# Performance work log

Measured on AMD Instinct MI355X. Metric: run time of the kernel, lower is better.

Reference implementation:

```python
import jax, jax.numpy as jnp
import numpy as np

N_NODES = 50000
N_EDGES = 1_600_000
N_HEADS = 8
IN_DIM = 512
OUT_DIM = 64
LRELU_ALPHA = 0.2


def setup_inputs() -> dict:
    key = jax.random.key(0)
    k1, k2, k3, k4, k5 = jax.random.split(key, 5)
    x = jax.random.normal(k1, (N_NODES, IN_DIM), dtype=jnp.float32)
    # glorot-ish scale for weights
    W = jax.random.normal(k2, (N_HEADS, IN_DIM, OUT_DIM), dtype=jnp.float32) * (1.0 / np.sqrt(IN_DIM))
    att_w = jax.random.normal(k3, (N_HEADS, 2 * OUT_DIM), dtype=jnp.float32) * (1.0 / np.sqrt(2 * OUT_DIM))
    src = jax.random.randint(k4, (N_EDGES,), 0, N_NODES, dtype=jnp.int64 if jax.config.read('jax_enable_x64') else jnp.int32).astype(jnp.int32)
    dst = jax.random.randint(k5, (N_EDGES,), 0, N_NODES, dtype=jnp.int32)
    return {"x": x, "W": W, "att_w": att_w, "src": src, "dst": dst}


def reference(x, W, att_w, src, dst):
    # GAT forward (eval mode: dropout=0, bias off, heads concatenated).
    # attention score: leaky_relu([f_src || f_dst] @ a) == leaky_relu(a1.f_src + a2.f_dst)
    outs = []
    for h in range(N_HEADS):
        feat = x @ W[h]                               # [N, F]
        a1 = att_w[h, :OUT_DIM]                       # [F]
        a2 = att_w[h, OUT_DIM:]                       # [F]
        alpha_s = feat @ a1                           # [N]
        alpha_d = feat @ a2                           # [N]
        logit = jax.nn.leaky_relu(alpha_s[src] + alpha_d[dst], LRELU_ALPHA)  # [E]
        # sparse row-wise softmax over segments keyed by src (row index)
        m = jax.ops.segment_max(logit, src, num_segments=N_NODES)
        e = jnp.exp(logit - m[src])
        denom = jax.ops.segment_sum(e, src, num_segments=N_NODES)
        att = e / denom[src]                          # [E]
        # sparse-dense aggregation: out[row] = sum_edges att * feat[col]
        agg = jax.ops.segment_sum(att[:, None] * feat[dst], src, num_segments=N_NODES)  # [N, F]
        outs.append(jax.nn.relu(agg))                 # act per head (average_heads=False)
    return jnp.concatenate(outs, axis=1)              # [N, H*F]
```

## Files before the change

### kernel.cpp

```cpp
#include <hip/hip_runtime.h>
#include <math.h>

#define N_NODES   50000
#define N_EDGES   1600000
#define N_HEADS   8
#define IN_DIM    512
#define OUT_DIM   64
#define FEAT_DIM  512
#define LRELU_A   0.2f
#define M_TILES   391
#define M_PAD     (M_TILES*128)

#define DBLK_SHIFT 11
#define NBLK       25
#define NKEYS      (N_NODES * NBLK)
#define KSCAN_BLK  ((NKEYS + 1023) / 1024)

typedef __attribute__((ext_vector_type(8))) short bf16x8;
typedef __attribute__((ext_vector_type(4))) short bf16x4;
typedef __attribute__((ext_vector_type(4))) float f32x4;

__device__ inline unsigned short f2bf(float f) {
    unsigned int u = __float_as_uint(f);
    u = (u + 0x7FFFu + ((u >> 16) & 1u)) >> 16;
    return (unsigned short)u;
}
__device__ inline float bf2f(short s) {
    return __uint_as_float(((unsigned int)(unsigned short)s) << 16);
}

__global__ __launch_bounds__(256) void convert_x(const float* __restrict__ x,
                                                 unsigned short* __restrict__ xh) {
    int i = blockIdx.x * blockDim.x + threadIdx.x;
    if (i >= N_NODES * IN_DIM / 4) return;
    float4 v = ((const float4*)x)[i];
    ushort4 o;
    o.x = f2bf(v.x); o.y = f2bf(v.y); o.z = f2bf(v.z); o.w = f2bf(v.w);
    ((ushort4*)xh)[i] = o;
}

__global__ __launch_bounds__(256) void prep_b(const float* __restrict__ W,
                                              unsigned short* __restrict__ Bt) {
    int t = blockIdx.x * blockDim.x + threadIdx.x;
    if (t >= FEAT_DIM * IN_DIM) return;
    int n = t >> 9, k = t & 511;
    int h = n >> 6, o = n & 63;
    Bt[t] = f2bf(W[(size_t)h * IN_DIM * OUT_DIM + (size_t)k * OUT_DIM + o]);
}

__global__ __launch_bounds__(256) void gemm_mfma(const unsigned short* __restrict__ xh,
                                                 const unsigned short* __restrict__ Bt,
                                                 unsigned short* __restrict__ feat_h) {
    __shared__ __align__(16) unsigned short As[128 * 32];
    __shared__ __align__(16) unsigned short Bs[128 * 32];
    const int t    = threadIdx.x;
    const int wid  = t >> 6;
    const int lane = t & 63;
    const int m0   = blockIdx.x * 128;
    const int n0   = blockIdx.y * 128;
    const int wm   = (wid >> 1) * 64;
    const int wn   = (wid & 1) * 64;
    const int mr   = lane & 15;
    const int q    = lane >> 4;

    f32x4 acc[4][4];
    #pragma unroll
    for (int i = 0; i < 4; ++i)
        #pragma unroll
        for (int j = 0; j < 4; ++j) acc[i][j] = 0.0f;

    const char* xb = (const char*)xh;
    const char* bb = (const char*)Bt;
    const int o1 = t * 16;         const int row1 = o1 >> 6, kb1 = o1 & 63;
    const int o2 = t * 16 + 4096;  const int row2 = o2 >> 6, kb2 = o2 & 63;
    char* lA1 = ((char*)As) + wid * 1024;
    char* lA2 = ((char*)As) + 4096 + wid * 1024;
    char* lB1 = ((char*)Bs) + wid * 1024;
    char* lB2 = ((char*)Bs) + 4096 + wid * 1024;

    for (int k0 = 0; k0 < IN_DIM; k0 += 32) {
        const int kbyte = k0 * 2;
        __builtin_amdgcn_global_load_lds(
            (const __attribute__((address_space(1))) unsigned int*)(xb + (size_t)(m0 + row1) * (IN_DIM * 2) + kbyte + kb1),
            (__attribute__((address_space(3))) unsigned int*)lA1, 16, 0, 0);
        __builtin_amdgcn_global_load_lds(
            (const __attribute__((address_space(1))) unsigned int*)(xb + (size_t)(m0 + row2) * (IN_DIM * 2) + kbyte + kb2),
            (__attribute__((address_space(3))) unsigned int*)lA2, 16, 0, 0);
        __builtin_amdgcn_global_load_lds(
            (const __attribute__((address_space(1))) unsigned int*)(bb + (size_t)(n0 + row1) * (IN_DIM * 2) + kbyte + kb1),
            (__attribute__((address_space(3))) unsigned int*)lB1, 16, 0, 0);
        __builtin_amdgcn_global_load_lds(
            (const __attribute__((address_space(1))) unsigned int*)(bb + (size_t)(n0 + row2) * (IN_DIM * 2) + kbyte + kb2),
            (__attribute__((address_space(3))) unsigned int*)lB2, 16, 0, 0);
        __syncthreads();

        bf16x8 a[4], b[4];
        #pragma unroll
        for (int i = 0; i < 4; ++i)
            a[i] = *(const bf16x8*)&As[(wm + i * 16 + mr) * 32 + q * 8];
        #pragma unroll
        for (int j = 0; j < 4; ++j)
            b[j] = *(const bf16x8*)&Bs[(wn + j * 16 + mr) * 32 + q * 8];
        #pragma unroll
        for (int i = 0; i < 4; ++i)
            #pragma unroll
            for (int j = 0; j < 4; ++j)
                acc[i][j] = __builtin_amdgcn_mfma_f32_16x16x32_bf16(a[i], b[j], acc[i][j], 0, 0, 0);
        __syncthreads();
    }

    #pragma unroll
    for (int i = 0; i < 4; ++i) {
        #pragma unroll
        for (int j = 0; j < 4; ++j) {
            int col = n0 + wn + j * 16 + mr;
            #pragma unroll
            for (int r = 0; r < 4; ++r) {
                int row = m0 + wm + i * 16 + q * 4 + r;
                if (row < N_NODES)
                    feat_h[(size_t)row * FEAT_DIM + col] = f2bf(acc[i][j][r]);
            }
        }
    }
}

__global__ __launch_bounds__(256) void alpha_kernel(const unsigned short* __restrict__ feat_h,
                                                    const float* __restrict__ att_w,
                                                    float* __restrict__ alpha_s,
                                                    float* __restrict__ alpha_d) {
    int node = (blockIdx.x * blockDim.x + threadIdx.x) >> 6;
    int lane = threadIdx.x & 63;
    if (node >= N_NODES) return;
    int h   = lane >> 3;
    int sub = lane & 7;
    bf16x8 f = *(const bf16x8*)&feat_h[(size_t)node * FEAT_DIM + lane * 8];
    float s = 0.f, d = 0.f;
    #pragma unroll
    for (int i = 0; i < 8; ++i) {
        float fv = bf2f(f[i]);
        s += fv * att_w[h * 128 + sub * 8 + i];
        d += fv * att_w[h * 128 + 64 + sub * 8 + i];
    }
    #pragma unroll
    for (int off = 1; off < 8; off <<= 1) {
        s += __shfl_xor(s, off);
        d += __shfl_xor(d, off);
    }
    if (sub == 0) {
        alpha_s[node * N_HEADS + h] = s;
        alpha_d[node * N_HEADS + h] = d;
    }
}

__global__ __launch_bounds__(256) void count_kernel(const int* __restrict__ src,
                                                    const int* __restrict__ dst,
                                                    int* __restrict__ cnt) {
    int e = (blockIdx.x * blockDim.x + threadIdx.x) * 4;
    if (e < N_EDGES) {
        int4 s = *(const int4*)&src[e];
        int4 d = *(const int4*)&dst[e];
        atomicAdd(&cnt[s.x * NBLK + (d.x >> DBLK_SHIFT)], 1);
        atomicAdd(&cnt[s.y * NBLK + (d.y >> DBLK_SHIFT)], 1);
        atomicAdd(&cnt[s.z * NBLK + (d.z >> DBLK_SHIFT)], 1);
        atomicAdd(&cnt[s.w * NBLK + (d.w >> DBLK_SHIFT)], 1);
    }
}

__global__ __launch_bounds__(1024) void scan_block_sums(const int* __restrict__ cnt,
                                                        int* __restrict__ partials) {
    __shared__ int wsum[16];
    const int t    = threadIdx.x;
    const int lane = t & 63;
    const int wid  = t >> 6;
    int i = blockIdx.x * 1024 + t;
    int v = (i < NKEYS) ? cnt[i] : 0;
    #pragma unroll
    for (int off = 32; off > 0; off >>= 1) v += __shfl_xor(v, off);
    if (lane == 0) wsum[wid] = v;
    __syncthreads();
    if (t < 16) {
        int u = wsum[t];
        #pragma unroll
        for (int off = 1; off < 16; off <<= 1) u += __shfl_xor(u, off);
        if (t == 0) partials[blockIdx.x] = u;
    }
}

__global__ __launch_bounds__(1024) void scan_partials(const int* __restrict__ partials,
                                                      int* __restrict__ blkoff,
                                                      int* __restrict__ keyptr) {
    __shared__ int wsum[16];
    const int t    = threadIdx.x;
    const int lane = t & 63;
    const int wid  = t >> 6;
    int carry = 0;
    for (int base = 0; base < KSCAN_BLK; base += 1024) {
        int i = base + t;
        int v = (i < KSCAN_BLK) ? partials[i] : 0;
        int incl = v;
        #pragma unroll
        for (int off = 1; off < 64; off <<= 1) {
            int u = __shfl_up(incl, off);
            if (lane >= off) incl += u;
        }
        if (lane == 63) wsum[wid] = incl;
        __syncthreads();
        if (t < 16) {
            int u = wsum[t];
            #pragma unroll
            for (int off = 1; off < 16; off <<= 1) {
                int w = __shfl_up(u, off);
                if (t >= off) u += w;
            }
            wsum[t] = u;
        }
        __syncthreads();
        int woff = (wid > 0) ? wsum[wid - 1] : 0;
        if (i < KSCAN_BLK) blkoff[i] = carry + woff + incl - v;
        carry += wsum[15];
        __syncthreads();
    }
    if (t == 0) keyptr[NKEYS] = carry;
}

__global__ __launch_bounds__(1024) void scan_apply(const int* __restrict__ cnt,
                                                   const int* __restrict__ blkoff,
                                                   int* __restrict__ keyptr,
                                                   int* __restrict__ cursor) {
    __shared__ int wsum[16];
    const int t    = threadIdx.x;
    const int lane = t & 63;
    const int wid  = t >> 6;
    int i = blockIdx.x * 1024 + t;
    int v = (i < NKEYS) ? cnt[i] : 0;
    int incl = v;
    #pragma unroll
    for (int off = 1; off < 64; off <<= 1) {
        int u = __shfl_up(incl, off);
        if (lane >= off) incl += u;
    }
    if (lane == 63) wsum[wid] = incl;
    __syncthreads();
    if (t < 16) {
        int u = wsum[t];
        #pragma unroll
        for (int off = 1; off < 16; off <<= 1) {
            int w = __shfl_up(u, off);
            if (t >= off) u += w;
        }
        wsum[t] = u;
    }
    __syncthreads();
    int woff = (wid > 0) ? wsum[wid - 1] : 0;
    int excl = blkoff[blockIdx.x] + woff + incl - v;
    if (i < NKEYS) { keyptr[i] = excl; cursor[i] = excl; }
}

__global__ __launch_bounds__(256) void scatter_kernel(const int* __restrict__ src,
                                                      const int* __restrict__ dst,
                                                      int* __restrict__ cursor,
                                                      int* __restrict__ csr_dst) {
    int e = (blockIdx.x * blockDim.x + threadIdx.x) * 4;
    if (e < N_EDGES) {
        int4 s = *(const int4*)&src[e];
        int4 d = *(const int4*)&dst[e];
        int p0 = atomicAdd(&cursor[s.x * NBLK + (d.x >> DBLK_SHIFT)], 1); csr_dst[p0] = d.x;
        int p1 = atomicAdd(&cursor[s.y * NBLK + (d.y >> DBLK_SHIFT)], 1); csr_dst[p1] = d.y;
        int p2 = atomicAdd(&cursor[s.z * NBLK + (d.z >> DBLK_SHIFT)], 1); csr_dst[p2] = d.z;
        int p3 = atomicAdd(&cursor[s.w * NBLK + (d.w >> DBLK_SHIFT)], 1); csr_dst[p3] = d.w;
    }
}

__global__ __launch_bounds__(256) void agg_kernel(const unsigned short* __restrict__ feat_h,
                                                  const float* __restrict__ alpha_s,
                                                  const float* __restrict__ alpha_d,
                                                  const int* __restrict__ keyptr,
                                                  const int* __restrict__ csr_dst,
                                                  float* __restrict__ out,
                                                  int hg) {
    __shared__ float red[2][64][5];
    const int wv   = __builtin_amdgcn_readfirstlane(threadIdx.x >> 6);
    const int lane = threadIdx.x & 63;
    const int node = blockIdx.x * 2 + (wv >> 1);
    const int half = wv & 1;
    const int h    = hg * 4 + (lane >> 4);

    const int start = keyptr[node * NBLK];
    const int end   = keyptr[node * NBLK + NBLK];
    const int deg   = end - start;
    const int lo    = start + ((deg * half) >> 1);
    const int hi    = start + ((deg * (half + 1)) >> 1);
    const int cnt2  = hi - lo;
    const float as  = alpha_s[node * N_HEADS + h];
    const int* cd   = csr_dst + lo;
    const unsigned short* fb = feat_h + hg * 256 + lane * 4;

    float sacc = 0.f;
    float acc[4] = {};

    int j = 0;
    for (; j + 16 <= cnt2; j += 16) {
        int d[16];
        #pragma unroll
        for (int k = 0; k < 16; ++k) d[k] = cd[j + k];
        float ad[16];
        #pragma unroll
        for (int k = 0; k < 16; ++k) ad[k] = alpha_d[(size_t)d[k] * N_HEADS + h];
        bf16x4 f[16];
        #pragma unroll
        for (int k = 0; k < 16; ++k)
            f[k] = *(const bf16x4*)&fb[(size_t)d[k] * FEAT_DIM];
        float e[16];
        #pragma unroll
        for (int k = 0; k < 16; ++k) {
            float z = as + ad[k];
            z = z > 0.f ? z : LRELU_A * z;
            e[k] = __expf(z);
        }
        float s0 = 0.f;
        #pragma unroll
        for (int k = 0; k < 16; ++k) s0 += e[k];
        sacc += s0;
        #pragma unroll
        for (int i = 0; i < 4; ++i) {
            float a = acc[i];
            #pragma unroll
            for (int k = 0; k < 16; ++k) a += e[k] * bf2f(f[k][i]);
            acc[i] = a;
        }
    }
    for (; j + 4 <= cnt2; j += 4) {
        int d[4];
        #pragma unroll
        for (int k = 0; k < 4; ++k) d[k] = cd[j + k];
        float ad[4];
        #pragma unroll
        for (int k = 0; k < 4; ++k) ad[k] = alpha_d[(size_t)d[k] * N_HEADS + h];
        bf16x4 f[4];
        #pragma unroll
        for (int k = 0; k < 4; ++k)
            f[k] = *(const bf16x4*)&fb[(size_t)d[k] * FEAT_DIM];
        float e[4];
        #pragma unroll
        for (int k = 0; k < 4; ++k) {
            float z = as + ad[k];
            z = z > 0.f ? z : LRELU_A * z;
            e[k] = __expf(z);
        }
        sacc += (e[0] + e[1]) + (e[2] + e[3]);
        #pragma unroll
        for (int i = 0; i < 4; ++i) {
            float a = acc[i];
            #pragma unroll
            for (int k = 0; k < 4; ++k) a += e[k] * bf2f(f[k][i]);
            acc[i] = a;
        }
    }
    for (; j < cnt2; ++j) {
        int dd = cd[j];
        float ad0 = alpha_d[(size_t)dd * N_HEADS + h];
        bf16x4 f0 = *(const bf16x4*)&fb[(size_t)dd * FEAT_DIM];
        float z = as + ad0; z = z > 0.f ? z : LRELU_A * z;
        float e0 = __expf(z);
        sacc += e0;
        #pragma unroll
        for (int i = 0; i < 4; ++i) acc[i] += e0 * bf2f(f0[i]);
    }

    const int pr = wv >> 1;
    if (half == 1) {
        #pragma unroll
        for (int i = 0; i < 4; ++i) red[pr][lane][i] = acc[i];
        red[pr][lane][4] = sacc;
    }
    __syncthreads();
    if (half == 0) {
        #pragma unroll
        for (int i = 0; i < 4; ++i) acc[i] += red[pr][lane][i];
        sacc += red[pr][lane][4];
        const float inv = (deg > 0) ? 1.f / sacc : 0.f;
        f32x4 o0 = { fmaxf(acc[0] * inv, 0.f), fmaxf(acc[1] * inv, 0.f),
                     fmaxf(acc[2] * inv, 0.f), fmaxf(acc[3] * inv, 0.f) };
        f32x4* op = (f32x4*)(out + (size_t)node * FEAT_DIM + hg * 256 + lane * 4);
        __builtin_nontemporal_store(o0, op);
    }
}

extern "C" void kernel_launch(void* const* d_in, const int* in_sizes, int n_in,
                              void* d_out, int out_size, void* d_ws, size_t ws_size,
                              hipStream_t stream) {
    const float* x     = (const float*)d_in[0];
    const float* W     = (const float*)d_in[1];
    const float* att_w = (const float*)d_in[2];
    const int*   src   = (const int*)d_in[3];
    const int*   dst   = (const int*)d_in[4];
    float* out = (float*)d_out;

    char* ws = (char*)d_ws;
    size_t off = 0;
    auto alloc = [&](size_t bytes) {
        void* p = ws + off;
        off += (bytes + 255) & ~(size_t)255;
        return p;
    };
    unsigned short* feat_h = (unsigned short*)alloc((size_t)N_NODES * FEAT_DIM * sizeof(short));
    unsigned short* xh     = (unsigned short*)alloc((size_t)M_PAD * IN_DIM * sizeof(short));
    unsigned short* Bt     = (unsigned short*)alloc((size_t)FEAT_DIM * IN_DIM * sizeof(short));
    float* alpha_s = (float*)alloc((size_t)N_NODES * N_HEADS * sizeof(float));
    float* alpha_d = (float*)alloc((size_t)N_NODES * N_HEADS * sizeof(float));
    int*   cnt     = (int*)alloc((size_t)NKEYS * sizeof(int));
    int*   keyptr  = (int*)alloc((size_t)(NKEYS + 1) * sizeof(int));
    int*   csr_dst = (int*)alloc((size_t)N_EDGES * sizeof(int));
    int*   partials = (int*)alloc((size_t)KSCAN_BLK * sizeof(int));
    int*   blkoff   = (int*)alloc((size_t)KSCAN_BLK * sizeof(int));
    int*   cursor   = cnt;

    (void)hipMemsetAsync(cnt, 0, (size_t)NKEYS * sizeof(int), stream);

    convert_x<<<(N_NODES * IN_DIM / 4 + 255) / 256, 256, 0, stream>>>(x, xh);
    prep_b<<<(FEAT_DIM * IN_DIM + 255) / 256, 256, 0, stream>>>(W, Bt);

    dim3 ggrid(M_TILES, FEAT_DIM / 128);
    gemm_mfma<<<ggrid, 256, 0, stream>>>(xh, Bt, feat_h);

    alpha_kernel<<<(N_NODES + 3) / 4, 256, 0, stream>>>(feat_h, att_w, alpha_s, alpha_d);

    count_kernel<<<(N_EDGES / 4 + 255) / 256, 256, 0, stream>>>(src, dst, cnt);
    scan_block_sums<<<KSCAN_BLK, 1024, 0, stream>>>(cnt, partials);
    scan_partials<<<1, 1024, 0, stream>>>(partials, blkoff, keyptr);
    scan_apply<<<KSCAN_BLK, 1024, 0, stream>>>(cnt, blkoff, keyptr, cursor);
    scatter_kernel<<<(N_EDGES / 4 + 255) / 256, 256, 0, stream>>>(src, dst, cursor, csr_dst);

    agg_kernel<<<N_NODES / 2, 256, 0, stream>>>(feat_h, alpha_s, alpha_d, keyptr, csr_dst, out, 0);
    agg_kernel<<<N_NODES / 2, 256, 0, stream>>>(feat_h, alpha_s, alpha_d, keyptr, csr_dst, out, 1);
}
```

Measured before the change: 685.8 us.

## Fuse edge counting into conversion and CSR scatter into GEMM launch

Folds the edge-count atomics into the x-to-bf16 conversion kernel and the CSR scatter atomics into the MFMA GEMM kernel by interleaving block roles within one grid. The scan is moved ahead of the GEMM so the scatter blocks can run alongside the GEMM tiles. This removes kernel launches and aims to hide atomic latency under bandwidth- and compute-bound work. It risks contention and uneven block scheduling, and the GEMM grid is linearized differently, which may change cache locality.

```diff
diff --git a/kernel.cpp b/kernel.cpp
--- a/kernel.cpp
+++ b/kernel.cpp
@@ -16,6 +16,10 @@
 #define NKEYS      (N_NODES * NBLK)
 #define KSCAN_BLK  ((NKEYS + 1023) / 1024)
 
+#define EDGE_BLK   782
+#define CVT_BLK    25000
+#define GEMM_TILES 1564
+
 typedef __attribute__((ext_vector_type(8))) short bf16x8;
 typedef __attribute__((ext_vector_type(4))) short bf16x4;
 typedef __attribute__((ext_vector_type(4))) float f32x4;
@@ -29,9 +33,33 @@
     return __uint_as_float(((unsigned int)(unsigned short)s) << 16);
 }
 
-__global__ __launch_bounds__(256) void convert_x(const float* __restrict__ x,
-                                                 unsigned short* __restrict__ xh) {
-    int i = blockIdx.x * blockDim.x + threadIdx.x;
+__global__ __launch_bounds__(256) void convert_count(const float* __restrict__ x,
+                                                     unsigned short* __restrict__ xh,
+                                                     const int* __restrict__ src,
+                                                     const int* __restrict__ dst,
+                                                     int* __restrict__ cnt) {
+    const int id = blockIdx.x;
+    if (id < 2 * EDGE_BLK && (id & 1)) {
+        const int blk = id >> 1;
+        const int e = (blk * 256 + threadIdx.x) * 8;
+        if (e < N_EDGES) {
+            int4 s0 = *(const int4*)&src[e];
+            int4 s1 = *(const int4*)&src[e + 4];
+            int4 d0 = *(const int4*)&dst[e];
+            int4 d1 = *(const int4*)&dst[e + 4];
+            atomicAdd(&cnt[s0.x * NBLK + (d0.x >> DBLK_SHIFT)], 1);
+            atomicAdd(&cnt[s0.y * NBLK + (d0.y >> DBLK_SHIFT)], 1);
+            atomicAdd(&cnt[s0.z * NBLK + (d0.z >> DBLK_SHIFT)], 1);
+            atomicAdd(&cnt[s0.w * NBLK + (d0.w >> DBLK_SHIFT)], 1);
+            atomicAdd(&cnt[s1.x * NBLK + (d1.x >> DBLK_SHIFT)], 1);
+            atomicAdd(&cnt[s1.y * NBLK + (d1.y >> DBLK_SHIFT)], 1);
+            atomicAdd(&cnt[s1.z * NBLK + (d1.z >> DBLK_SHIFT)], 1);
+            atomicAdd(&cnt[s1.w * NBLK + (d1.w >> DBLK_SHIFT)], 1);
+        }
+        return;
+    }
+    const int c = (id < 2 * EDGE_BLK) ? (id >> 1) : (id - EDGE_BLK);
+    const int i = c * 256 + threadIdx.x;
     if (i >= N_NODES * IN_DIM / 4) return;
     float4 v = ((const float4*)x)[i];
     ushort4 o;
@@ -48,16 +76,52 @@
     Bt[t] = f2bf(W[(size_t)h * IN_DIM * OUT_DIM + (size_t)k * OUT_DIM + o]);
 }
 
-__global__ __launch_bounds__(256) void gemm_mfma(const unsigned short* __restrict__ xh,
-                                                 const unsigned short* __restrict__ Bt,
-                                                 unsigned short* __restrict__ feat_h) {
+__global__ __launch_bounds__(256) void gemm_scatter(const unsigned short* __restrict__ xh,
+                                                    const unsigned short* __restrict__ Bt,
+                                                    unsigned short* __restrict__ feat_h,
+                                                    const int* __restrict__ src,
+                                                    const int* __restrict__ dst,
+                                                    int* __restrict__ cursor,
+                                                    int* __restrict__ csr_dst) {
     __shared__ __align__(16) unsigned short As[128 * 32];
     __shared__ __align__(16) unsigned short Bs[128 * 32];
+    const unsigned id = blockIdx.x;
+    const unsigned q3 = id / 3u;
+    const unsigned r3 = id - q3 * 3u;
+
+    if (r3 == 2u) {
+        const int e = ((int)q3 * 256 + (int)threadIdx.x) * 8;
+        if (e < N_EDGES) {
+            int4 s0 = *(const int4*)&src[e];
+            int4 s1 = *(const int4*)&src[e + 4];
+            int4 d0 = *(const int4*)&dst[e];
+            int4 d1 = *(const int4*)&dst[e + 4];
+            int p0 = atomicAdd(&cursor[s0.x * NBLK + (d0.x >> DBLK_SHIFT)], 1);
+            int p1 = atomicAdd(&cursor[s0.y * NBLK + (d0.y >> DBLK_SHIFT)], 1);
+            int p2 = atomicAdd(&cursor[s0.z * NBLK + (d0.z >> DBLK_SHIFT)], 1);
+            int p3 = atomicAdd(&cursor[s0.w * NBLK + (d0.w >> DBLK_SHIFT)], 1);
+            int p4 = atomicAdd(&cursor[s1.x * NBLK + (d1.x >> DBLK_SHIFT)], 1);
+            int p5 = atomicAdd(&cursor[s1.y * NBLK + (d1.y >> DBLK_SHIFT)], 1);
+            int p6 = atomicAdd(&cursor[s1.z * NBLK + (d1.z >> DBLK_SHIFT)], 1);
+            int p7 = atomicAdd(&cursor[s1.w * NBLK + (d1.w >> DBLK_SHIFT)], 1);
+            csr_dst[p0] = d0.x;
+            csr_dst[p1] = d0.y;
+            csr_dst[p2] = d0.z;
+            csr_dst[p3] = d0.w;
+            csr_dst[p4] = d1.x;
+            csr_dst[p5] = d1.y;
+            csr_dst[p6] = d1.z;
+            csr_dst[p7] = d1.w;
+        }
+        return;
+    }
+
+    const unsigned g = q3 * 2u + r3;
     const int t    = threadIdx.x;
     const int wid  = t >> 6;
     const int lane = t & 63;
-    const int m0   = blockIdx.x * 128;
-    const int n0   = blockIdx.y * 128;
+    const int m0   = (int)(g >> 2) * 128;
+    const int n0   = (int)(g & 3u) * 128;
     const int wm   = (wid >> 1) * 64;
     const int wn   = (wid & 1) * 64;
     const int mr   = lane & 15;
@@ -152,20 +216,6 @@
     }
 }
 
-__global__ __launch_bounds__(256) void count_kernel(const int* __restrict__ src,
-                                                    const int* __restrict__ dst,
-                                                    int* __restrict__ cnt) {
-    int e = (blockIdx.x * blockDim.x + threadIdx.x) * 4;
-    if (e < N_EDGES) {
-        int4 s = *(const int4*)&src[e];
-        int4 d = *(const int4*)&dst[e];
-        atomicAdd(&cnt[s.x * NBLK + (d.x >> DBLK_SHIFT)], 1);
-        atomicAdd(&cnt[s.y * NBLK + (d.y >> DBLK_SHIFT)], 1);
-        atomicAdd(&cnt[s.z * NBLK + (d.z >> DBLK_SHIFT)], 1);
-        atomicAdd(&cnt[s.w * NBLK + (d.w >> DBLK_SHIFT)], 1);
-    }
-}
-
 __global__ __launch_bounds__(1024) void scan_block_sums(const int* __restrict__ cnt,
                                                         int* __restrict__ partials) {
     __shared__ int wsum[16];
@@ -254,21 +304,6 @@
     int woff = (wid > 0) ? wsum[wid - 1] : 0;
     int excl = blkoff[blockIdx.x] + woff + incl - v;
     if (i < NKEYS) { keyptr[i] = excl; cursor[i] = excl; }
-}
-
-__global__ __launch_bounds__(256) void scatter_kernel(const int* __restrict__ src,
-                                                      const int* __restrict__ dst,
-                                                      int* __restrict__ cursor,
-                                                      int* __restrict__ csr_dst) {
-    int e = (blockIdx.x * blockDim.x + threadIdx.x) * 4;
-    if (e < N_EDGES) {
-        int4 s = *(const int4*)&src[e];
-        int4 d = *(const int4*)&dst[e];
-        int p0 = atomicAdd(&cursor[s.x * NBLK + (d.x >> DBLK_SHIFT)], 1); csr_dst[p0] = d.x;
-        int p1 = atomicAdd(&cursor[s.y * NBLK + (d.y >> DBLK_SHIFT)], 1); csr_dst[p1] = d.y;
-        int p2 = atomicAdd(&cursor[s.z * NBLK + (d.z >> DBLK_SHIFT)], 1); csr_dst[p2] = d.z;
-        int p3 = atomicAdd(&cursor[s.w * NBLK + (d.w >> DBLK_SHIFT)], 1); csr_dst[p3] = d.w;
-    }
 }
 
 __global__ __launch_bounds__(256) void agg_kernel(const unsigned short* __restrict__ feat_h,
@@ -417,19 +452,16 @@
 
     (void)hipMemsetAsync(cnt, 0, (size_t)NKEYS * sizeof(int), stream);
 
-    convert_x<<<(N_NODES * IN_DIM / 4 + 255) / 256, 256, 0, stream>>>(x, xh);
+    convert_count<<<CVT_BLK + EDGE_BLK, 256, 0, stream>>>(x, xh, src, dst, cnt);
     prep_b<<<(FEAT_DIM * IN_DIM + 255) / 256, 256, 0, stream>>>(W, Bt);
 
-    dim3 ggrid(M_TILES, FEAT_DIM / 128);
-    gemm_mfma<<<ggrid, 256, 0, stream>>>(xh, Bt, feat_h);
-
-    alpha_kernel<<<(N_NODES + 3) / 4, 256, 0, stream>>>(feat_h, att_w, alpha_s, alpha_d);
-
-    count_kernel<<<(N_EDGES / 4 + 255) / 256, 256, 0, stream>>>(src, dst, cnt);
     scan_block_sums<<<KSCAN_BLK, 1024, 0, stream>>>(cnt, partials);
     scan_partials<<<1, 1024, 0, stream>>>(partials, blkoff, keyptr);
     scan_apply<<<KSCAN_BLK, 1024, 0, stream>>>(cnt, blkoff, keyptr, cursor);
-    scatter_kernel<<<(N_EDGES / 4 + 255) / 256, 256, 0, stream>>>(src, dst, cursor, csr_dst);
+
+    gemm_scatter<<<3 * EDGE_BLK, 256, 0, stream>>>(xh, Bt, feat_h, src, dst, cursor, csr_dst);
+
+    alpha_kernel<<<(N_NODES + 3) / 4, 256, 0, stream>>>(feat_h, att_w, alpha_s, alpha_d);
 
     agg_kernel<<<N_NODES / 2, 256, 0, stream>>>(feat_h, alpha_s, alpha_d, keyptr, csr_dst, out, 0);
     agg_kernel<<<N_NODES / 2, 256, 0, stream>>>(feat_h, alpha_s, alpha_d, keyptr, csr_dst, out, 1);
```

Measured after the change: 598.0 us. 12.8% less time.
